# Kernel optimization log

Hardware: AMD Instinct MI355X
Metric: run time of the kernel (lower is better)

## Reference

```python
import jax, jax.numpy as jnp
import numpy as np

D, H, K = 384, 6, 8

def _ln(x, g, b, eps=1e-5):
    mu = jnp.mean(x, axis=-1, keepdims=True)
    var = jnp.mean((x - mu) ** 2, axis=-1, keepdims=True)
    return (x - mu) * jax.lax.rsqrt(var + eps) * g + b

def setup_inputs() -> dict:
    key = jax.random.key(0)
    ks = jax.random.split(key, 20)
    B, N = 4, 2048
    s = 0.02
    inp = {
        'x': jax.random.normal(ks[0], (B, N, D), jnp.float32),
        'knn_index': jax.random.randint(ks[1], (B * K * N,), 0, B * N, jnp.int64),
        'ln1_g': jnp.ones((D,), jnp.float32),
        'ln1_b': jnp.zeros((D,), jnp.float32),
        'w_qkv': jax.random.normal(ks[2], (D, 3 * D), jnp.float32) * s,
        'w_proj': jax.random.normal(ks[3], (D, D), jnp.float32) * s,
        'b_proj': jnp.zeros((D,), jnp.float32),
        'w_knn': jax.random.normal(ks[4], (2 * D, D), jnp.float32) * s,
        'b_knn': jnp.zeros((D,), jnp.float32),
        'w_g1': jax.random.normal(ks[5], (2 * D, D), jnp.float32) * s,
        'b_g1': jnp.zeros((D,), jnp.float32),
        'w_g2': jax.random.normal(ks[6], (D, D), jnp.float32) * s,
        'b_g2': jnp.zeros((D,), jnp.float32),
        'ln2_g': jnp.ones((D,), jnp.float32),
        'ln2_b': jnp.zeros((D,), jnp.float32),
        'w_fc1': jax.random.normal(ks[7], (D, 4 * D), jnp.float32) * s,
        'b_fc1': jnp.zeros((4 * D,), jnp.float32),
        'w_fc2': jax.random.normal(ks[8], (4 * D, D), jnp.float32) * s,
        'b_fc2': jnp.zeros((D,), jnp.float32),
    }
    return inp

def reference(x, knn_index, ln1_g, ln1_b, w_qkv, w_proj, b_proj, w_knn, b_knn,
              w_g1, b_g1, w_g2, b_g2, ln2_g, ln2_b, w_fc1, b_fc1, w_fc2, b_fc2):
    B, N, _ = x.shape
    hd = D // H
    scale = hd ** -0.5
    nx = _ln(x, ln1_g, ln1_b)
    # --- self attention ---
    qkv = (nx @ w_qkv).reshape(B, N, 3, H, hd).transpose(2, 0, 3, 1, 4)  # [3,B,H,N,hd]
    q, k, v = qkv[0], qkv[1], qkv[2]
    attn = jax.nn.softmax(jnp.einsum('bhnd,bhmd->bhnm', q * scale, k), axis=-1)
    attn_out = jnp.einsum('bhnm,bhmd->bhnd', attn, v).transpose(0, 2, 1, 3).reshape(B, N, D)
    attn_out = attn_out @ w_proj + b_proj
    # --- EdgeConv-style graph feature: gather-concat-MLP-maxpool ---
    feat = nx.reshape(B * N, D)[knn_index].reshape(B, K, N, D)
    xe = jnp.broadcast_to(nx[:, None], (B, K, N, D))
    gf = jnp.concatenate([feat - xe, xe], axis=-1)  # [B,K,N,2D]
    knn_out = jnp.max(jax.nn.leaky_relu(gf @ w_knn + b_knn, 0.2), axis=1)  # [B,N,D]
    # --- salience gate ---
    gi = jnp.concatenate([attn_out, knn_out], axis=-1)
    gate = jax.nn.sigmoid(jax.nn.gelu(gi @ w_g1 + b_g1, approximate=False) @ w_g2 + b_g2)
    fused = (1 - gate) * attn_out + gate * knn_out
    x = x + fused
    # --- FFN ---
    h = jax.nn.gelu(_ln(x, ln2_g, ln2_b) @ w_fc1 + b_fc1, approximate=False)
    x = x + (h @ w_fc2 + b_fc2)
    return x
```

## Files before the change

### kernel.cpp

```cpp
#include <hip/hip_runtime.h>
#include <math.h>

typedef unsigned short u16;
typedef __attribute__((ext_vector_type(8))) short short8;
typedef __attribute__((ext_vector_type(4))) float floatx4;
typedef __attribute__((ext_vector_type(4))) short sh4v;

union sh4u { sh4v v; u16 u[4]; };
union sh8u { short8 v; u16 u[8]; };

__device__ __forceinline__ floatx4 mfma16(short8 a, short8 b, floatx4 c) {
  return __builtin_amdgcn_mfma_f32_16x16x32_bf16(a, b, c, 0, 0, 0);
}

__device__ __forceinline__ floatx4 zero4() {
  floatx4 z = {0.f, 0.f, 0.f, 0.f};
  return z;
}

__device__ __forceinline__ u16 f2b(float f) {
  union { float f; unsigned u; } v; v.f = f;
  unsigned u = v.u;
  return (u16)((u + 0x7FFFu + ((u >> 16) & 1u)) >> 16);
}

__device__ __forceinline__ float b2f(u16 u) {
  union { unsigned u; float f; } v; v.u = ((unsigned)u) << 16;
  return v.f;
}

__device__ __forceinline__ float gelu_exact(float x) {
  return 0.5f * x * (1.f + erff(x * 0.70710678118654752440f));
}

__device__ __forceinline__ unsigned pack2(float a, float b) {
  return (unsigned)f2b(a) | ((unsigned)f2b(b) << 16);
}

__device__ __forceinline__ unsigned permpack(float p0, float p1) {
  return __builtin_amdgcn_perm(__float_as_uint(p1), __float_as_uint(p0), 0x07060302u);
}

__global__ __launch_bounds__(256) void tcln_kernel(
    const float* __restrict__ p0, const float* __restrict__ p1,
    const float* __restrict__ p2, const float* __restrict__ p3,
    const float* __restrict__ p4, const float* __restrict__ p5,
    const float* __restrict__ wknn,
    u16* __restrict__ o0, u16* __restrict__ o1, u16* __restrict__ o2,
    u16* __restrict__ o3, u16* __restrict__ o4, u16* __restrict__ o5,
    u16* __restrict__ wcT,
    const float* __restrict__ x, const float* __restrict__ g,
    const float* __restrict__ bia, u16* __restrict__ nx) {
  __shared__ u16 L[64][66];
  int t = blockIdx.x, tid = threadIdx.x;
  if (t >= 612) {
    int wave = tid >> 6, lane = tid & 63;
    int row = (t - 612) * 4 + wave;
    const float* xr = x + (size_t)row * 384;
    float v[6];
    float s = 0.f;
#pragma unroll
    for (int j = 0; j < 6; j++) { v[j] = xr[lane + 64 * j]; s += v[j]; }
#pragma unroll
    for (int off = 32; off > 0; off >>= 1) s += __shfl_xor(s, off);
    float mu = s * (1.f / 384.f);
    float ss = 0.f;
#pragma unroll
    for (int j = 0; j < 6; j++) { float d = v[j] - mu; ss += d * d; }
#pragma unroll
    for (int off = 32; off > 0; off >>= 1) ss += __shfl_xor(ss, off);
    float rstd = rsqrtf(ss * (1.f / 384.f) + 1e-5f);
    u16* orow = nx + (size_t)row * 384;
#pragma unroll
    for (int j = 0; j < 6; j++) {
      int d = lane + 64 * j;
      orow[d] = f2b((v[j] - mu) * rstd * g[d] + bia[d]);
    }
    return;
  }
  if (t >= 540) {
    t -= 540;
    int tk = t / 12, tn = t % 12;
    int k0 = tk * 64, j0 = tn * 64;
#pragma unroll
    for (int i = 0; i < 4; i++) {
      int c = tid + 256 * i;
      int r = c >> 4, c4 = (c & 15) * 4;
      floatx4 v;
      if (j0 < 384) {
        v = *(const floatx4*)(wknn + (size_t)(k0 + r) * 384 + j0 + c4);
      } else {
        floatx4 a = *(const floatx4*)(wknn + (size_t)(384 + k0 + r) * 384 + (j0 - 384) + c4);
        floatx4 b = *(const floatx4*)(wknn + (size_t)(k0 + r) * 384 + (j0 - 384) + c4);
        v = a - b;
      }
      *(unsigned*)&L[r][c4]     = pack2(v[0], v[1]);
      *(unsigned*)&L[r][c4 + 2] = pack2(v[2], v[3]);
    }
    __syncthreads();
#pragma unroll
    for (int i = 0; i < 2; i++) {
      int c = tid + 256 * i;
      int nn = c >> 3, k8 = (c & 7) * 8;
      sh8u pk;
#pragma unroll
      for (int j = 0; j < 8; j++) pk.u[j] = L[k8 + j][nn];
      *(short8*)(wcT + (size_t)(j0 + nn) * 384 + k0 + k8) = pk.v;
    }
    return;
  }
  const float* src; u16* dst; int Kd, Nd, tk, tn;
  if      (t < 108) { src = p0; dst = o0; Kd = 384;  Nd = 1152; tk = t / 18; tn = t % 18; }
  else if (t < 144) { src = p1; dst = o1; Kd = 384;  Nd = 384;  t -= 108; tk = t / 6;  tn = t % 6; }
  else if (t < 216) { src = p2; dst = o2; Kd = 768;  Nd = 384;  t -= 144; tk = t / 6;  tn = t % 6; }
  else if (t < 252) { src = p3; dst = o3; Kd = 384;  Nd = 384;  t -= 216; tk = t / 6;  tn = t % 6; }
  else if (t < 396) { src = p4; dst = o4; Kd = 384;  Nd = 1536; t -= 252; tk = t / 24; tn = t % 24; }
  else              { src = p5; dst = o5; Kd = 1536; Nd = 384;  t -= 396; tk = t / 6;  tn = t % 6; }
  int k0 = tk * 64, n0 = tn * 64;
#pragma unroll
  for (int i = 0; i < 4; i++) {
    int c = tid + 256 * i;
    int r = c >> 4, c4 = (c & 15) * 4;
    floatx4 v = *(const floatx4*)(src + (size_t)(k0 + r) * Nd + n0 + c4);
    *(unsigned*)&L[r][c4]     = pack2(v[0], v[1]);
    *(unsigned*)&L[r][c4 + 2] = pack2(v[2], v[3]);
  }
  __syncthreads();
#pragma unroll
  for (int i = 0; i < 2; i++) {
    int c = tid + 256 * i;
    int nn = c >> 3, k8 = (c & 7) * 8;
    sh8u pk;
#pragma unroll
    for (int j = 0; j < 8; j++) pk.u[j] = L[k8 + j][nn];
    *(short8*)(dst + (size_t)(n0 + nn) * Kd + k0 + k8) = pk.v;
  }
}

__global__ __launch_bounds__(256) void lnb_kernel(const u16* __restrict__ x,
                                                  const float* __restrict__ g,
                                                  const float* __restrict__ bia,
                                                  u16* __restrict__ out) {
  int wave = threadIdx.x >> 6, lane = threadIdx.x & 63;
  int row = blockIdx.x * 4 + wave;
  const u16* xr = x + (size_t)row * 384;
  float v[6];
  float s = 0.f;
#pragma unroll
  for (int j = 0; j < 6; j++) { v[j] = b2f(xr[lane + 64 * j]); s += v[j]; }
#pragma unroll
  for (int off = 32; off > 0; off >>= 1) s += __shfl_xor(s, off);
  float mu = s * (1.f / 384.f);
  float ss = 0.f;
#pragma unroll
  for (int j = 0; j < 6; j++) { float d = v[j] - mu; ss += d * d; }
#pragma unroll
  for (int off = 32; off > 0; off >>= 1) ss += __shfl_xor(ss, off);
  float rstd = rsqrtf(ss * (1.f / 384.f) + 1e-5f);
  u16* orow = out + (size_t)row * 384;
#pragma unroll
  for (int j = 0; j < 6; j++) {
    int d = lane + 64 * j;
    orow[d] = f2b((v[j] - mu) * rstd * g[d] + bia[d]);
  }
}

template <int EPI>
__global__ __launch_bounds__(256) void gemm64_kernel(
    const u16* __restrict__ A0, const u16* __restrict__ A1, int Ksplit,
    const u16* __restrict__ BwT, const u16* __restrict__ BwT2, int N, int K,
    const float* __restrict__ bias,
    float* __restrict__ outF, u16* __restrict__ outB, u16* __restrict__ outB2,
    const u16* __restrict__ eA16, const u16* __restrict__ eK16,
    const float* __restrict__ eX, u16* __restrict__ outV) {
  __shared__ u16 As[64][72];
  __shared__ u16 Bs[128][72];
  int tid = threadIdx.x;
  int lane = tid & 63, w = tid >> 6, quad = lane >> 4, l16 = lane & 15;
  int n0 = blockIdx.x * 128, m0 = blockIdx.y * 64;
  int ra = tid >> 3, ca = (tid & 7) * 8;
  const u16* Bsrc = BwT;
  int nbase = n0;
  if (EPI == 8 && n0 >= 1152) { Bsrc = BwT2; nbase = n0 - 1152; }
  floatx4 acc[4][2];
#pragma unroll
  for (int i = 0; i < 4; i++)
#pragma unroll
    for (int j = 0; j < 2; j++) acc[i][j] = zero4();

  short8 pa[2], pb[4];
  auto loadAB = [&](int k0) {
    const u16* Ap;
    int kk, sA;
    if (k0 < Ksplit) { Ap = A0; kk = k0; sA = Ksplit; }
    else             { Ap = A1; kk = k0 - Ksplit; sA = K - Ksplit; }
    pa[0] = *(const short8*)(Ap + (size_t)(m0 + ra) * sA + kk + ca);
    pa[1] = *(const short8*)(Ap + (size_t)(m0 + ra + 32) * sA + kk + ca);
#pragma unroll
    for (int i = 0; i < 4; i++)
      pb[i] = *(const short8*)(Bsrc + (size_t)(nbase + ra + 32 * i) * K + k0 + ca);
  };
  loadAB(0);
  int iters = K >> 6;
  for (int kt = 0; kt < iters; kt++) {
    __syncthreads();
    *(short8*)&As[ra][ca] = pa[0];
    *(short8*)&As[ra + 32][ca] = pa[1];
#pragma unroll
    for (int i = 0; i < 4; i++) *(short8*)&Bs[ra + 32 * i][ca] = pb[i];
    __syncthreads();
    if (kt + 1 < iters) loadAB((kt + 1) * 64);
#pragma unroll
    for (int kh = 0; kh < 2; kh++) {
      short8 af[4], bfr[2];
#pragma unroll
      for (int mt = 0; mt < 4; mt++)
        af[mt] = *(const short8*)&As[mt * 16 + l16][kh * 32 + quad * 8];
#pragma unroll
      for (int nt = 0; nt < 2; nt++)
        bfr[nt] = *(const short8*)&Bs[w * 32 + nt * 16 + l16][kh * 32 + quad * 8];
#pragma unroll
      for (int mt = 0; mt < 4; mt++)
#pragma unroll
        for (int nt = 0; nt < 2; nt++)
          acc[mt][nt] = mfma16(af[mt], bfr[nt], acc[mt][nt]);
    }
  }

#pragma unroll
  for (int mt = 0; mt < 4; mt++)
#pragma unroll
    for (int nt = 0; nt < 2; nt++) {
      int col = n0 + w * 32 + nt * 16 + l16;
      int row0 = m0 + mt * 16 + quad * 4;
      if (EPI == 8) {
        if (col < 1152) {
          float sc = (col < 384) ? 0.18033688011112042f : 1.f;
          sh4u pk;
#pragma unroll
          for (int r = 0; r < 4; r++) {
            u16 bv = f2b(acc[mt][nt][r] * sc);
            outB[(size_t)(row0 + r) * 1152 + col] = bv;
            pk.u[r] = bv;
          }
          if (col >= 768) {
            int b = row0 >> 11, n = row0 & 2047;
            int hd = col - 768;
            *(sh4v*)(outV + ((size_t)(b * 6 + (hd >> 6)) * 64 + (hd & 63)) * 2048 + n) = pk.v;
          }
        } else {
#pragma unroll
          for (int r = 0; r < 4; r++)
            outB2[(size_t)(row0 + r) * 768 + (col - 1152)] = f2b(acc[mt][nt][r]);
        }
      } else {
#pragma unroll
        for (int r = 0; r < 4; r++) {
          size_t rc = (size_t)(row0 + r) * N + col;
          float v = acc[mt][nt][r];
          if (EPI == 3) {
            outB[rc] = f2b(gelu_exact(v + bias[col]));
          } else if (EPI == 4) {
            float gte = 1.f / (1.f + __expf(-(v + bias[col])));
            float fu = (1.f - gte) * b2f(eA16[rc]) + gte * b2f(eK16[rc]);
            outB[rc] = f2b(eX[rc] + fu);
          } else if (EPI == 7) {
            outF[rc] = v + bias[col] + b2f(eA16[rc]);
          }
        }
      }
    }
}

__global__ __launch_bounds__(256) void attnknn_kernel(
    const u16* __restrict__ qkv, const u16* __restrict__ Vt,
    u16* __restrict__ OPb, float* __restrict__ LS,
    const u16* __restrict__ GBb, const int* __restrict__ kidx,
    const float* __restrict__ bknn, u16* __restrict__ knn_bf) {
  __shared__ u16 Ks[64][72];
  __shared__ u16 Vts[64][72];
  __shared__ u16 Ps[4][32][72];
  int bid = blockIdx.x, tid = threadIdx.x;
  int lane = tid & 63, w = tid >> 6, quad = lane >> 4, l16 = lane & 15;
  if (bid >= 1536) {
    int row = (bid - 1536) * 4 + w;
    int b = row >> 11, n = row & 2047;
    float base[6], acc[6];
#pragma unroll
    for (int j = 0; j < 6; j++) {
      int d = lane + 64 * j;
      base[j] = b2f(GBb[(size_t)row * 768 + 384 + d]) + bknn[d];
      acc[j] = -1e30f;
    }
    for (int kk = 0; kk < 8; kk++) {
      int g = kidx[(b * 8 + kk) * 2048 + n];
      const u16* Gr = GBb + (size_t)g * 768;
#pragma unroll
      for (int j = 0; j < 6; j++) {
        float v = b2f(Gr[lane + 64 * j]) + base[j];
        v = v > 0.f ? v : 0.2f * v;
        acc[j] = fmaxf(acc[j], v);
      }
    }
#pragma unroll
    for (int j = 0; j < 6; j++)
      knn_bf[(size_t)row * 384 + lane + 64 * j] = f2b(acc[j]);
    return;
  }
  int split = bid / 384;
  int rr = bid - split * 384;
  int bh = rr >> 4, b = bh / 6, h = bh % 6;
  int q0 = (rr & 15) * 128;
  const u16* qbase = qkv + (size_t)b * 2048 * 1152 + h * 64;
  const u16* kbase = qbase + 384 + (size_t)split * 512 * 1152;
  const u16* vtb = Vt + (size_t)bh * 64 * 2048 + split * 512;
  short8 qf[2][2];
#pragma unroll
  for (int s = 0; s < 2; s++) {
    int qrow = q0 + w * 32 + s * 16 + l16;
    qf[s][0] = *(const short8*)(qbase + (size_t)qrow * 1152 + quad * 8);
    qf[s][1] = *(const short8*)(qbase + (size_t)qrow * 1152 + 32 + quad * 8);
  }
  short8 ones;
#pragma unroll
  for (int j = 0; j < 8; j++) ones[j] = (short)0x3F80;
  floatx4 O[4][2];
  floatx4 accL[2] = {zero4(), zero4()};
#pragma unroll
  for (int i = 0; i < 4; i++)
#pragma unroll
    for (int s = 0; s < 2; s++) O[i][s] = zero4();

  int rb = tid >> 3, c8 = (tid & 7) * 8;
  short8 rk[2], rv[2];
  rk[0] = *(const short8*)(kbase + (size_t)rb * 1152 + c8);
  rk[1] = *(const short8*)(kbase + (size_t)(rb + 32) * 1152 + c8);
  rv[0] = *(const short8*)(vtb + (size_t)rb * 2048 + c8);
  rv[1] = *(const short8*)(vtb + (size_t)(rb + 32) * 2048 + c8);

  for (int kt = 0; kt < 8; kt++) {
    __syncthreads();
    *(short8*)&Ks[rb][c8] = rk[0];
    *(short8*)&Ks[rb + 32][c8] = rk[1];
    *(short8*)&Vts[rb][c8] = rv[0];
    *(short8*)&Vts[rb + 32][c8] = rv[1];
    __syncthreads();
    if (kt < 7) {
      int key0 = (kt + 1) * 64;
      rk[0] = *(const short8*)(kbase + (size_t)(key0 + rb) * 1152 + c8);
      rk[1] = *(const short8*)(kbase + (size_t)(key0 + rb + 32) * 1152 + c8);
      rv[0] = *(const short8*)(vtb + (size_t)rb * 2048 + key0 + c8);
      rv[1] = *(const short8*)(vtb + (size_t)(rb + 32) * 2048 + key0 + c8);
    }
#pragma unroll
    for (int mt = 0; mt < 4; mt++) {
      short8 k0 = *(const short8*)&Ks[mt * 16 + l16][quad * 8];
      short8 k1 = *(const short8*)&Ks[mt * 16 + l16][32 + quad * 8];
#pragma unroll
      for (int s = 0; s < 2; s++) {
        floatx4 st = mfma16(k0, qf[s][0], zero4());
        st = mfma16(k1, qf[s][1], st);
        uint2 pk;
        pk.x = permpack(exp2f(st[0]), exp2f(st[1]));
        pk.y = permpack(exp2f(st[2]), exp2f(st[3]));
        *(uint2*)&Ps[w][s * 16 + l16][mt * 16 + quad * 4] = pk;
      }
    }
    short8 pf[2][2];
#pragma unroll
    for (int s = 0; s < 2; s++) {
      pf[s][0] = *(const short8*)&Ps[w][s * 16 + l16][quad * 8];
      pf[s][1] = *(const short8*)&Ps[w][s * 16 + l16][32 + quad * 8];
      accL[s] = mfma16(ones, pf[s][0], accL[s]);
      accL[s] = mfma16(ones, pf[s][1], accL[s]);
    }
#pragma unroll
    for (int mt2 = 0; mt2 < 4; mt2++) {
      short8 v0 = *(const short8*)&Vts[mt2 * 16 + l16][quad * 8];
      short8 v1 = *(const short8*)&Vts[mt2 * 16 + l16][32 + quad * 8];
#pragma unroll
      for (int s = 0; s < 2; s++) {
        O[mt2][s] = mfma16(v0, pf[s][0], O[mt2][s]);
        O[mt2][s] = mfma16(v1, pf[s][1], O[mt2][s]);
      }
    }
  }
#pragma unroll
  for (int s = 0; s < 2; s++) {
    int row = b * 2048 + q0 + w * 32 + s * 16 + l16;
    u16* orow = OPb + (size_t)split * 8192 * 384 + (size_t)row * 384 + h * 64;
#pragma unroll
    for (int mt2 = 0; mt2 < 4; mt2++) {
      sh4u pk;
#pragma unroll
      for (int r = 0; r < 4; r++) pk.u[r] = f2b(O[mt2][s][r]);
      *(sh4v*)(orow + mt2 * 16 + quad * 4) = pk.v;
    }
    if (quad == 0) LS[split * 8192 + row] = accL[s][0];
  }
}

__global__ __launch_bounds__(256) void projc_kernel(
    const u16* __restrict__ OPb, const float* __restrict__ LS,
    const u16* __restrict__ BwT, const float* __restrict__ bias,
    u16* __restrict__ outB) {
  __shared__ u16 As[64][72];
  __shared__ u16 Bs[128][72];
  int tid = threadIdx.x;
  int lane = tid & 63, w = tid >> 6, quad = lane >> 4, l16 = lane & 15;
  int n0 = blockIdx.x * 128, m0 = blockIdx.y * 64;
  int ra = tid >> 3, ca = (tid & 7) * 8;
  const size_t SP = (size_t)8192 * 384;
  floatx4 acc[4][2];
#pragma unroll
  for (int i = 0; i < 4; i++)
#pragma unroll
    for (int j = 0; j < 2; j++) acc[i][j] = zero4();

  short8 pa[2], pb[4];
  auto loadAB = [&](int k0) {
#pragma unroll
    for (int i = 0; i < 2; i++) {
      const u16* p = OPb + (size_t)(m0 + ra + 32 * i) * 384 + k0 + ca;
      sh8u a0, a1, a2, a3, pk;
      a0.v = *(const short8*)p;
      a1.v = *(const short8*)(p + SP);
      a2.v = *(const short8*)(p + 2 * SP);
      a3.v = *(const short8*)(p + 3 * SP);
#pragma unroll
      for (int j = 0; j < 8; j++)
        pk.u[j] = f2b((b2f(a0.u[j]) + b2f(a1.u[j])) + (b2f(a2.u[j]) + b2f(a3.u[j])));
      pa[i] = pk.v;
    }
#pragma unroll
    for (int i = 0; i < 4; i++)
      pb[i] = *(const short8*)(BwT + (size_t)(n0 + ra + 32 * i) * 384 + k0 + ca);
  };
  loadAB(0);
  for (int kt = 0; kt < 6; kt++) {
    __syncthreads();
    *(short8*)&As[ra][ca] = pa[0];
    *(short8*)&As[ra + 32][ca] = pa[1];
#pragma unroll
    for (int i = 0; i < 4; i++) *(short8*)&Bs[ra + 32 * i][ca] = pb[i];
    __syncthreads();
    if (kt < 5) loadAB((kt + 1) * 64);
#pragma unroll
    for (int kh = 0; kh < 2; kh++) {
      short8 af[4], bfr[2];
#pragma unroll
      for (int mt = 0; mt < 4; mt++)
        af[mt] = *(const short8*)&As[mt * 16 + l16][kh * 32 + quad * 8];
#pragma unroll
      for (int nt = 0; nt < 2; nt++)
        bfr[nt] = *(const short8*)&Bs[w * 32 + nt * 16 + l16][kh * 32 + quad * 8];
#pragma unroll
      for (int mt = 0; mt < 4; mt++)
#pragma unroll
        for (int nt = 0; nt < 2; nt++)
          acc[mt][nt] = mfma16(af[mt], bfr[nt], acc[mt][nt]);
    }
  }
#pragma unroll
  for (int mt = 0; mt < 4; mt++) {
    int row0 = m0 + mt * 16 + quad * 4;
    float rl[4];
#pragma unroll
    for (int r = 0; r < 4; r++) {
      int gr = row0 + r;
      rl[r] = 1.f / ((LS[gr] + LS[8192 + gr]) + (LS[16384 + gr] + LS[24576 + gr]));
    }
#pragma unroll
    for (int nt = 0; nt < 2; nt++) {
      int col = n0 + w * 32 + nt * 16 + l16;
#pragma unroll
      for (int r = 0; r < 4; r++)
        outB[(size_t)(row0 + r) * 384 + col] = f2b(acc[mt][nt][r] * rl[r] + bias[col]);
    }
  }
}

extern "C" void kernel_launch(void* const* d_in, const int* in_sizes, int n_in,
                              void* d_out, int out_size, void* d_ws, size_t ws_size,
                              hipStream_t stream) {
  const float* x    = (const float*)d_in[0];
  const int* kidx   = (const int*)d_in[1];
  const float* ln1g = (const float*)d_in[2];
  const float* ln1b = (const float*)d_in[3];
  const float* wqkv = (const float*)d_in[4];
  const float* wproj= (const float*)d_in[5];
  const float* bproj= (const float*)d_in[6];
  const float* wknn = (const float*)d_in[7];
  const float* bknn = (const float*)d_in[8];
  const float* wg1  = (const float*)d_in[9];
  const float* bg1  = (const float*)d_in[10];
  const float* wg2  = (const float*)d_in[11];
  const float* bg2  = (const float*)d_in[12];
  const float* ln2g = (const float*)d_in[13];
  const float* ln2b = (const float*)d_in[14];
  const float* wfc1 = (const float*)d_in[15];
  const float* bfc1 = (const float*)d_in[16];
  const float* wfc2 = (const float*)d_in[17];
  const float* bfc2 = (const float*)d_in[18];
  float* out = (float*)d_out;

  const int M = 8192;
  char* ws = (char*)d_ws;
  size_t off = 0;
  auto alloc = [&](size_t bytes) -> char* {
    char* p = ws + off;
    off += (bytes + 255) & ~(size_t)255;
    return p;
  };
  u16* nx_bf    = (u16*)alloc((size_t)M * 384 * 2);
  u16* qkv_bf   = (u16*)alloc((size_t)M * 1152 * 2);
  u16* attn_bf  = (u16*)alloc((size_t)M * 384 * 2);
  u16* GBb      = (u16*)alloc((size_t)M * 768 * 2);
  u16* knn_bf   = (u16*)alloc((size_t)M * 384 * 2);
  u16* x2b      = (u16*)alloc((size_t)M * 384 * 2);
  u16* t1_bf    = (u16*)alloc((size_t)M * 384 * 2);
  u16* nx2_bf   = (u16*)alloc((size_t)M * 384 * 2);
  u16* Vt_b     = (u16*)alloc((size_t)24 * 64 * 2048 * 2);
  u16* OPb      = (u16*)alloc((size_t)4 * M * 384 * 2);
  float* LS     = (float*)alloc((size_t)4 * M * 4);
  u16* wqkvT    = (u16*)alloc((size_t)1152 * 384 * 2);
  u16* wprojT   = (u16*)alloc(384 * 384 * 2);
  u16* wcT      = (u16*)alloc((size_t)768 * 384 * 2);
  u16* wg1T     = (u16*)alloc((size_t)384 * 768 * 2);
  u16* wg2T     = (u16*)alloc(384 * 384 * 2);
  u16* wfc1T    = (u16*)alloc((size_t)1536 * 384 * 2);
  u16* wfc2T    = (u16*)alloc((size_t)384 * 1536 * 2);
  u16* h_bf     = qkv_bf;

  tcln_kernel<<<2660, 256, 0, stream>>>(wqkv, wproj, wg1, wg2, wfc1, wfc2, wknn,
                                        wqkvT, wprojT, wg1T, wg2T, wfc1T, wfc2T, wcT,
                                        x, ln1g, ln1b, nx_bf);
  gemm64_kernel<8><<<dim3(15, 128), 256, 0, stream>>>(nx_bf, nx_bf, 384, wqkvT, wcT, 1920, 384,
                                                      nullptr, nullptr, qkv_bf, GBb,
                                                      nullptr, nullptr, nullptr, Vt_b);
  attnknn_kernel<<<3584, 256, 0, stream>>>(qkv_bf, Vt_b, OPb, LS,
                                           GBb, kidx, bknn, knn_bf);
  projc_kernel<<<dim3(3, 128), 256, 0, stream>>>(OPb, LS, wprojT, bproj, attn_bf);
  gemm64_kernel<3><<<dim3(3, 128), 256, 0, stream>>>(attn_bf, knn_bf, 384, wg1T, nullptr, 384, 768,
                                                     bg1, nullptr, t1_bf, nullptr,
                                                     nullptr, nullptr, nullptr, nullptr);
  gemm64_kernel<4><<<dim3(3, 128), 256, 0, stream>>>(t1_bf, t1_bf, 384, wg2T, nullptr, 384, 384,
                                                     bg2, nullptr, x2b, nullptr,
                                                     attn_bf, knn_bf, x, nullptr);
  lnb_kernel<<<2048, 256, 0, stream>>>(x2b, ln2g, ln2b, nx2_bf);
  gemm64_kernel<3><<<dim3(12, 128), 256, 0, stream>>>(nx2_bf, nx2_bf, 384, wfc1T, nullptr, 1536, 384,
                                                      bfc1, nullptr, h_bf, nullptr,
                                                      nullptr, nullptr, nullptr, nullptr);
  gemm64_kernel<7><<<dim3(3, 128), 256, 0, stream>>>(h_bf, h_bf, 1536, wfc2T, nullptr, 384, 1536,
                                                     bfc2, out, nullptr, nullptr,
                                                     x2b, nullptr, nullptr, nullptr);
  (void)in_sizes; (void)n_in; (void)out_size; (void)ws_size;
}
```

Measured before the change: 277.1 us.

## Use 32x32 MFMA with permlane swap in attention, vectorize knn gather-max

The attention loop moves from 16x16x32 to 32x32x16 bf16 MFMA tiles and builds the P operand in registers with permlane32 swaps, which removes the per-wave Ps shared-memory round trip. Block IDs are remapped so that consecutive blocks spread across splits. The knn gather-max branch is also restructured: it preloads the eight indices, loads packed bf16 pairs, takes the max before adding the bias and before the leaky-relu (valid because both are monotone), and writes packed outputs. This costs more accumulator registers per wave and relies on a gfx950-specific builtin.

```diff
diff --git a/kernel.cpp b/kernel.cpp
--- a/kernel.cpp
+++ b/kernel.cpp
@@ -4,17 +4,29 @@
 typedef unsigned short u16;
 typedef __attribute__((ext_vector_type(8))) short short8;
 typedef __attribute__((ext_vector_type(4))) float floatx4;
+typedef __attribute__((ext_vector_type(16))) float floatx16;
 typedef __attribute__((ext_vector_type(4))) short sh4v;
+typedef __attribute__((ext_vector_type(2))) unsigned uint2v;
 
 union sh4u { sh4v v; u16 u[4]; };
 union sh8u { short8 v; u16 u[8]; };
+union sh8w { short8 v; unsigned w[4]; };
 
 __device__ __forceinline__ floatx4 mfma16(short8 a, short8 b, floatx4 c) {
   return __builtin_amdgcn_mfma_f32_16x16x32_bf16(a, b, c, 0, 0, 0);
 }
+__device__ __forceinline__ floatx16 mfma32(short8 a, short8 b, floatx16 c) {
+  return __builtin_amdgcn_mfma_f32_32x32x16_bf16(a, b, c, 0, 0, 0);
+}
 
 __device__ __forceinline__ floatx4 zero4() {
   floatx4 z = {0.f, 0.f, 0.f, 0.f};
+  return z;
+}
+__device__ __forceinline__ floatx16 zero16() {
+  floatx16 z;
+#pragma unroll
+  for (int i = 0; i < 16; i++) z[i] = 0.f;
   return z;
 }
 
@@ -26,6 +38,15 @@
 
 __device__ __forceinline__ float b2f(u16 u) {
   union { unsigned u; float f; } v; v.u = ((unsigned)u) << 16;
+  return v.f;
+}
+
+__device__ __forceinline__ float blo(unsigned w) {
+  union { unsigned u; float f; } v; v.u = w << 16;
+  return v.f;
+}
+__device__ __forceinline__ float bhi(unsigned w) {
+  union { unsigned u; float f; } v; v.u = w & 0xFFFF0000u;
   return v.f;
 }
 
@@ -279,57 +300,71 @@
     const float* __restrict__ bknn, u16* __restrict__ knn_bf) {
   __shared__ u16 Ks[64][72];
   __shared__ u16 Vts[64][72];
-  __shared__ u16 Ps[4][32][72];
   int bid = blockIdx.x, tid = threadIdx.x;
-  int lane = tid & 63, w = tid >> 6, quad = lane >> 4, l16 = lane & 15;
+  int lane = tid & 63, w = tid >> 6;
   if (bid >= 1536) {
     int row = (bid - 1536) * 4 + w;
     int b = row >> 11, n = row & 2047;
-    float base[6], acc[6];
-#pragma unroll
-    for (int j = 0; j < 6; j++) {
-      int d = lane + 64 * j;
-      base[j] = b2f(GBb[(size_t)row * 768 + 384 + d]) + bknn[d];
-      acc[j] = -1e30f;
-    }
+    const unsigned* browp = (const unsigned*)(GBb + (size_t)row * 768 + 384);
+    uint2v bw01 = *(const uint2v*)(browp + 2 * lane);
+    unsigned bw2 = browp[128 + lane];
+    floatx4 bk4 = *(const floatx4*)(bknn + 4 * lane);
+    float bk40 = bknn[256 + 2 * lane], bk41 = bknn[256 + 2 * lane + 1];
+    int gi[8];
+#pragma unroll
+    for (int kk = 0; kk < 8; kk++) gi[kk] = kidx[(b * 8 + kk) * 2048 + n];
+    float mx[6];
+#pragma unroll
+    for (int e = 0; e < 6; e++) mx[e] = -1e30f;
+#pragma unroll
     for (int kk = 0; kk < 8; kk++) {
-      int g = kidx[(b * 8 + kk) * 2048 + n];
-      const u16* Gr = GBb + (size_t)g * 768;
-#pragma unroll
-      for (int j = 0; j < 6; j++) {
-        float v = b2f(Gr[lane + 64 * j]) + base[j];
-        v = v > 0.f ? v : 0.2f * v;
-        acc[j] = fmaxf(acc[j], v);
-      }
-    }
-#pragma unroll
-    for (int j = 0; j < 6; j++)
-      knn_bf[(size_t)row * 384 + lane + 64 * j] = f2b(acc[j]);
+      const unsigned* gp = (const unsigned*)(GBb + (size_t)gi[kk] * 768);
+      uint2v g01 = *(const uint2v*)(gp + 2 * lane);
+      unsigned g2 = gp[128 + lane];
+      mx[0] = fmaxf(mx[0], blo(g01[0]));
+      mx[1] = fmaxf(mx[1], bhi(g01[0]));
+      mx[2] = fmaxf(mx[2], blo(g01[1]));
+      mx[3] = fmaxf(mx[3], bhi(g01[1]));
+      mx[4] = fmaxf(mx[4], blo(g2));
+      mx[5] = fmaxf(mx[5], bhi(g2));
+    }
+    float vv[6];
+    vv[0] = mx[0] + blo(bw01[0]) + bk4[0];
+    vv[1] = mx[1] + bhi(bw01[0]) + bk4[1];
+    vv[2] = mx[2] + blo(bw01[1]) + bk4[2];
+    vv[3] = mx[3] + bhi(bw01[1]) + bk4[3];
+    vv[4] = mx[4] + blo(bw2) + bk40;
+    vv[5] = mx[5] + bhi(bw2) + bk41;
+#pragma unroll
+    for (int e = 0; e < 6; e++) vv[e] = fmaxf(vv[e], 0.2f * vv[e]);
+    unsigned* op = (unsigned*)(knn_bf + (size_t)row * 384);
+    uint2v ow;
+    ow[0] = pack2(vv[0], vv[1]);
+    ow[1] = pack2(vv[2], vv[3]);
+    *(uint2v*)(op + 2 * lane) = ow;
+    op[128 + lane] = pack2(vv[4], vv[5]);
     return;
   }
-  int split = bid / 384;
-  int rr = bid - split * 384;
+  int vb = (bid & 7) * 192 + (bid >> 3);
+  int split = vb / 384;
+  int rr = vb - split * 384;
   int bh = rr >> 4, b = bh / 6, h = bh % 6;
   int q0 = (rr & 15) * 128;
+  int ql = lane & 31, h5 = lane >> 5;
   const u16* qbase = qkv + (size_t)b * 2048 * 1152 + h * 64;
   const u16* kbase = qbase + 384 + (size_t)split * 512 * 1152;
   const u16* vtb = Vt + (size_t)bh * 64 * 2048 + split * 512;
-  short8 qf[2][2];
-#pragma unroll
-  for (int s = 0; s < 2; s++) {
-    int qrow = q0 + w * 32 + s * 16 + l16;
-    qf[s][0] = *(const short8*)(qbase + (size_t)qrow * 1152 + quad * 8);
-    qf[s][1] = *(const short8*)(qbase + (size_t)qrow * 1152 + 32 + quad * 8);
-  }
+  int qrow = q0 + w * 32 + ql;
+  short8 qB[4];
+#pragma unroll
+  for (int s = 0; s < 4; s++)
+    qB[s] = *(const short8*)(qbase + (size_t)qrow * 1152 + s * 16 + h5 * 8);
   short8 ones;
 #pragma unroll
   for (int j = 0; j < 8; j++) ones[j] = (short)0x3F80;
-  floatx4 O[4][2];
-  floatx4 accL[2] = {zero4(), zero4()};
-#pragma unroll
-  for (int i = 0; i < 4; i++)
-#pragma unroll
-    for (int s = 0; s < 2; s++) O[i][s] = zero4();
+  floatx16 O[2];
+  O[0] = zero16(); O[1] = zero16();
+  floatx16 accL = zero16();
 
   int rb = tid >> 3, c8 = (tid & 7) * 8;
   short8 rk[2], rv[2];
@@ -353,51 +388,46 @@
       rv[1] = *(const short8*)(vtb + (size_t)(rb + 32) * 2048 + key0 + c8);
     }
 #pragma unroll
-    for (int mt = 0; mt < 4; mt++) {
-      short8 k0 = *(const short8*)&Ks[mt * 16 + l16][quad * 8];
-      short8 k1 = *(const short8*)&Ks[mt * 16 + l16][32 + quad * 8];
-#pragma unroll
-      for (int s = 0; s < 2; s++) {
-        floatx4 st = mfma16(k0, qf[s][0], zero4());
-        st = mfma16(k1, qf[s][1], st);
-        uint2 pk;
-        pk.x = permpack(exp2f(st[0]), exp2f(st[1]));
-        pk.y = permpack(exp2f(st[2]), exp2f(st[3]));
-        *(uint2*)&Ps[w][s * 16 + l16][mt * 16 + quad * 4] = pk;
+    for (int t = 0; t < 2; t++) {
+      floatx16 st = zero16();
+#pragma unroll
+      for (int s = 0; s < 4; s++) {
+        short8 aK = *(const short8*)&Ks[32 * t + ql][16 * s + 8 * h5];
+        st = mfma32(aK, qB[s], st);
       }
-    }
-    short8 pf[2][2];
-#pragma unroll
-    for (int s = 0; s < 2; s++) {
-      pf[s][0] = *(const short8*)&Ps[w][s * 16 + l16][quad * 8];
-      pf[s][1] = *(const short8*)&Ps[w][s * 16 + l16][32 + quad * 8];
-      accL[s] = mfma16(ones, pf[s][0], accL[s]);
-      accL[s] = mfma16(ones, pf[s][1], accL[s]);
-    }
-#pragma unroll
-    for (int mt2 = 0; mt2 < 4; mt2++) {
-      short8 v0 = *(const short8*)&Vts[mt2 * 16 + l16][quad * 8];
-      short8 v1 = *(const short8*)&Vts[mt2 * 16 + l16][32 + quad * 8];
-#pragma unroll
-      for (int s = 0; s < 2; s++) {
-        O[mt2][s] = mfma16(v0, pf[s][0], O[mt2][s]);
-        O[mt2][s] = mfma16(v1, pf[s][1], O[mt2][s]);
+      unsigned W[8];
+#pragma unroll
+      for (int j = 0; j < 8; j++)
+        W[j] = permpack(exp2f(st[2 * j]), exp2f(st[2 * j + 1]));
+#pragma unroll
+      for (int c = 0; c < 2; c++) {
+        int kk = 2 * t + c;
+        uint2v s0 = __builtin_amdgcn_permlane32_swap(W[4 * c], W[4 * c + 2], false, false);
+        uint2v s1 = __builtin_amdgcn_permlane32_swap(W[4 * c + 1], W[4 * c + 3], false, false);
+        sh8w pb_;
+        pb_.w[0] = s0[0];
+        pb_.w[1] = s1[0];
+        pb_.w[2] = s0[1];
+        pb_.w[3] = s1[1];
+        accL = mfma32(ones, pb_.v, accL);
+        short8 aV0 = *(const short8*)&Vts[ql][16 * kk + 8 * h5];
+        short8 aV1 = *(const short8*)&Vts[32 + ql][16 * kk + 8 * h5];
+        O[0] = mfma32(aV0, pb_.v, O[0]);
+        O[1] = mfma32(aV1, pb_.v, O[1]);
       }
     }
   }
-#pragma unroll
-  for (int s = 0; s < 2; s++) {
-    int row = b * 2048 + q0 + w * 32 + s * 16 + l16;
-    u16* orow = OPb + (size_t)split * 8192 * 384 + (size_t)row * 384 + h * 64;
-#pragma unroll
-    for (int mt2 = 0; mt2 < 4; mt2++) {
+  u16* orow = OPb + (size_t)split * 8192 * 384 + (size_t)(b * 2048 + qrow) * 384 + h * 64;
+#pragma unroll
+  for (int d = 0; d < 2; d++)
+#pragma unroll
+    for (int rq = 0; rq < 4; rq++) {
       sh4u pk;
 #pragma unroll
-      for (int r = 0; r < 4; r++) pk.u[r] = f2b(O[mt2][s][r]);
-      *(sh4v*)(orow + mt2 * 16 + quad * 4) = pk.v;
-    }
-    if (quad == 0) LS[split * 8192 + row] = accL[s][0];
-  }
+      for (int r3 = 0; r3 < 4; r3++) pk.u[r3] = f2b(O[d][4 * rq + r3]);
+      *(sh4v*)(orow + 32 * d + 8 * rq + 4 * h5) = pk.v;
+    }
+  if (lane < 32) LS[split * 8192 + b * 2048 + qrow] = accL[0];
 }
 
 __global__ __launch_bounds__(256) void projc_kernel(
```

New measurement: 267.6 us. -3.4%, faster.
